# Kernel tuning notes

Measured on AMD Instinct MI355X. Metric: run time of the kernel, lower is better.

Reference implementation:

```python
import jax, jax.numpy as jnp
import numpy as np

N, E = 50000, 800000
NFEAT, NHID, NCLASS = 512, 256, 64
RRELU_SLOPE = (1.0 / 8.0 + 1.0 / 3.0) / 2.0  # nn.RReLU eval-mode negative slope


def spmm(row, col, val, X):
    # sparse adj (COO: row, col, val) @ dense X -> [N, F]
    return jax.ops.segment_sum(X[col] * val[:, None], row, num_segments=N)


def setup_inputs() -> dict:
    key = jax.random.key(0)
    ks = jax.random.split(key, 12)
    x = jax.random.normal(ks[0], (N, NFEAT), dtype=jnp.float32)
    edge_row = jnp.sort(jax.random.randint(ks[1], (E,), 0, N))
    edge_col = jax.random.randint(ks[2], (E,), 0, N)
    # normalized-ish positive adjacency values
    edge_val = jax.random.uniform(ks[3], (E,), dtype=jnp.float32) / 16.0
    def glorot(k, fi, fo):
        s = 1.0 / np.sqrt(fi)
        return jax.random.normal(k, (fi, fo), dtype=jnp.float32) * s
    w1 = glorot(ks[4], NFEAT, NHID)
    b1 = jax.random.normal(ks[5], (NHID,), dtype=jnp.float32) * 0.01
    w2 = glorot(ks[6], NFEAT, NHID)
    b2 = jax.random.normal(ks[7], (NHID,), dtype=jnp.float32) * 0.01
    w3 = glorot(ks[8], NHID, NCLASS)
    b3 = jax.random.normal(ks[9], (NCLASS,), dtype=jnp.float32) * 0.01
    w4 = glorot(ks[10], NFEAT, NCLASS)
    b4 = jax.random.normal(ks[11], (NCLASS,), dtype=jnp.float32) * 0.01
    return {"x": x, "edge_row": edge_row, "edge_col": edge_col, "edge_val": edge_val,
            "w1": w1, "b1": b1, "w2": w2, "b2": b2, "w3": w3, "b3": b3, "w4": w4, "b4": b4}


def reference(x, edge_row, edge_col, edge_val, w1, b1, w2, b2, w3, b3, w4, b4):
    # skip branches (no adj): support = x @ W + b; dropout is identity in eval
    a_skip0 = x @ w2 + b2                                   # [N, NHID]
    a_skip1 = x @ w4 + b4                                   # [N, NCLASS]
    # gc1 with adj
    h1 = spmm(edge_row, edge_col, edge_val, x @ w1) + b1    # [N, NHID]
    v = h1 + a_skip0
    h = jnp.where(v >= 0, v, v * RRELU_SLOPE)               # RReLU (eval mode)
    # gc3 with adj
    out = spmm(edge_row, edge_col, edge_val, h @ w3) + b3 + a_skip1  # [N, NCLASS]
    return (out, w1, w2, w3, w4)
```

## Files before the change

kernel.cpp:

```cpp
#include <hip/hip_runtime.h>

#define N_NODES 50000
#define N_EDGES 800000
#define NFEAT 512
#define NHID 256
#define NCLASS 64
#define NCOMB 576
#define NPAD 640
#define NSKIP 320
#define RRELU_SLOPE 0.2291666666666667f

typedef __attribute__((ext_vector_type(8))) short bf16x8;
typedef __attribute__((ext_vector_type(4))) float f32x4;
typedef __attribute__((ext_vector_type(2))) float f32x2;

#define GLOAD_LDS16(g, l)                                                      \
    __builtin_amdgcn_global_load_lds(                                          \
        (const __attribute__((address_space(1))) void*)(g),                    \
        (__attribute__((address_space(3))) void*)(l), 16, 0, 0)

__device__ __forceinline__ unsigned short f2bf(float f) {
    unsigned int x = __float_as_uint(f);
    unsigned int r = (x + 0x7fffu + ((x >> 16) & 1u)) >> 16;
    return (unsigned short)r;
}
__device__ __forceinline__ float bf2f(unsigned short u) {
    return __uint_as_float(((unsigned int)u) << 16);
}
__device__ __forceinline__ float bf_lo(unsigned int u) { return __uint_as_float(u << 16); }
__device__ __forceinline__ float bf_hi(unsigned int u) { return __uint_as_float(u & 0xffff0000u); }
__device__ __forceinline__ unsigned char f2fp8(float v) {
    return (unsigned char)__builtin_amdgcn_cvt_pk_fp8_f32(v, v, 0, false);
}

#define P_BT 327680
#define P_TOT 328320
#define PK_BLK 1283
#define XC_BLK 2048
#define XC_N 6400000

__global__ __launch_bounds__(256)
void prep(const float* __restrict__ x, const float* __restrict__ w1,
          const float* __restrict__ w2, const float* __restrict__ w4,
          const float* __restrict__ b1, const float* __restrict__ b2,
          const float* __restrict__ b3, const float* __restrict__ b4,
          unsigned short* __restrict__ xb, unsigned short* __restrict__ Bt,
          float* __restrict__ biasb) {
    int b = blockIdx.x;
    if (b < PK_BLK) {
        int i = b * 256 + threadIdx.x;
        if (i < P_BT) {
            int c = i >> 9;
            int k = i & 511;
            float v = 0.f;
            if (c < NHID)            v = w1[k * NHID + c];
            else if (c < 2 * NHID)   v = w2[k * NHID + (c - NHID)];
            else if (c < NCOMB)      v = w4[k * NCLASS + (c - 2 * NHID)];
            Bt[i] = f2bf(v);
        } else if (i < P_TOT) {
            int bb = i - P_BT;
            float v = 0.f;
            if (bb >= NHID && bb < 2 * NHID)       v = b1[bb - NHID] + b2[bb - NHID];
            else if (bb >= 2 * NHID && bb < NCOMB) v = b3[bb - 2 * NHID] + b4[bb - 2 * NHID];
            biasb[bb] = v;
        }
        return;
    }
    for (int i = (b - PK_BLK) * 256 + threadIdx.x; i < XC_N; i += XC_BLK * 256) {
        float4 v = ((const float4*)x)[i];
        ushort4 o;
        o.x = f2bf(v.x); o.y = f2bf(v.y); o.z = f2bf(v.z); o.w = f2bf(v.w);
        ((ushort4*)xb)[i] = o;
    }
}

#define GBM 128
#define GBK 64
#define NCB0 5
#define NRP0 392
#define T0 800000
#define T1 850001
#define T2 866385
#define T3 944209
#define TAIL_BLOCKS ((T3 + 255) / 256)

__global__ __launch_bounds__(256, 4)
void gemm_bf16(const unsigned short* __restrict__ A,
               const unsigned short* __restrict__ Bt,
               const float* __restrict__ bias,
               unsigned char* __restrict__ C8,
               unsigned short* __restrict__ skipb,
               int M, int K,
               const int* __restrict__ erow, const int* __restrict__ ecol,
               const float* __restrict__ ev, const float* __restrict__ w1f,
               const float* __restrict__ w2f, const float* __restrict__ w3f,
               const float* __restrict__ w4f, uint2* __restrict__ ep,
               int* __restrict__ rp, unsigned short* __restrict__ w3t,
               float* __restrict__ outw) {
    __shared__ unsigned short As[GBM * GBK];
    __shared__ unsigned short Bs[128 * GBK];
    int row0, col0;
    {
        int b = blockIdx.x;
        if (b >= NRP0 * NCB0) {
            int i = (b - NRP0 * NCB0) * 256 + threadIdx.x;
            if (i < T0) {
                uint2 e;
                e.x = (unsigned)ecol[i];
                e.y = __float_as_uint(ev[i]);
                ep[i] = e;
            } else if (i < T1) {
                int n = i - T0;
                int lo = 0, hi = N_EDGES;
                while (lo < hi) {
                    int mid = (lo + hi) >> 1;
                    if (erow[mid] < n) lo = mid + 1; else hi = mid;
                }
                rp[n] = lo;
            } else if (i < T2) {
                int j = i - T1;
                int c = j >> 8;
                int k = j & 255;
                w3t[j] = f2bf(w3f[k * NCLASS + c]);
            } else if (i < T3) {
                int j = i - T2;
                float4* o4 = (float4*)outw;
                if (j < 32768)        o4[800000 + j] = ((const float4*)w1f)[j];
                else if (j < 65536)   o4[832768 + (j - 32768)] = ((const float4*)w2f)[j - 32768];
                else if (j < 69632)   o4[865536 + (j - 65536)] = ((const float4*)w3f)[j - 65536];
                else                  o4[869632 + (j - 69632)] = ((const float4*)w4f)[j - 69632];
            }
            return;
        }
        int g = b / (8 * NCB0);
        int w = b % (8 * NCB0);
        int r = g * 8 + (w & 7);
        int c = w >> 3;
        if (r * GBM >= M) return;
        row0 = r * GBM;
        col0 = c * 128;
    }
    const int tid  = threadIdx.x;
    const int lane = tid & 63;
    const int wave = tid >> 6;
    const int wr = (wave >> 1) * 64;
    const int wc = (wave & 1) * 64;
    const int lm = lane & 15;
    const int l4 = lane >> 4;
    const int sw = lm & 7;

    const int sub  = lane >> 3;
    const int slot = lane & 7;
    const int goct = slot ^ sub;

    f32x4 acc[4][4] = {};

    for (int k0 = 0; k0 < K; k0 += GBK) {
        #pragma unroll
        for (int p = 0; p < 4; ++p) {
            int chunk = wave * 4 + p;
            int gr = row0 + chunk * 8 + sub;
            if (gr > M - 1) gr = M - 1;
            GLOAD_LDS16(A + (size_t)gr * K + k0 + goct * 8, As + chunk * 512);
        }
        #pragma unroll
        for (int p = 0; p < 4; ++p) {
            int chunk = wave * 4 + p;
            int rb = col0 + chunk * 8 + sub;
            GLOAD_LDS16(Bt + (size_t)rb * K + k0 + goct * 8, Bs + chunk * 512);
        }
        __syncthreads();

        #pragma unroll
        for (int kk8 = 0; kk8 < GBK / 8; kk8 += 4) {
            const int so = ((kk8 + l4) ^ sw) * 8;
            bf16x8 bfr[4];
            #pragma unroll
            for (int j = 0; j < 4; ++j)
                bfr[j] = *(const bf16x8*)(Bs + (wc + j * 16 + lm) * 64 + so);
            #pragma unroll
            for (int i = 0; i < 4; ++i) {
                bf16x8 af = *(const bf16x8*)(As + (wr + i * 16 + lm) * 64 + so);
                #pragma unroll
                for (int j = 0; j < 4; ++j)
                    acc[i][j] = __builtin_amdgcn_mfma_f32_16x16x32_bf16(af, bfr[j], acc[i][j], 0, 0, 0);
            }
        }
        __syncthreads();
    }

    #pragma unroll
    for (int i = 0; i < 4; ++i) {
        #pragma unroll
        for (int j = 0; j < 4; ++j) {
            int col = col0 + wc + j * 16 + lm;
            float bvv = bias[col];
            #pragma unroll
            for (int r = 0; r < 4; ++r) {
                int row = row0 + wr + i * 16 + l4 * 4 + r;
                if (row < M) {
                    float v = acc[i][j][r];
                    if (col < NHID)       C8[(size_t)row * NHID + col] = f2fp8(v);
                    else if (col < NCOMB) skipb[(size_t)row * NSKIP + (col - NHID)] = f2bf(v + bvv);
                }
            }
        }
    }
}

__global__ __launch_bounds__(256)
void spmm1_rrelu_w3(const int* __restrict__ rp, const uint2* __restrict__ ep,
                    const unsigned char* __restrict__ xw1q,
                    const unsigned short* __restrict__ skipb,
                    const unsigned short* __restrict__ w3t,
                    unsigned char* __restrict__ hw3q, int n_nodes) {
    __shared__ unsigned short hs[16 * 256];
    const int tid = threadIdx.x;
    const int nb = blockIdx.x * 8;
    {
        uint4 z = {0u, 0u, 0u, 0u};
        ((uint4*)hs)[tid] = z;
        ((uint4*)hs)[256 + tid] = z;
    }
    __syncthreads();

    const int row = tid >> 5;
    const int n = nb + row;
    const int l = tid & 31;
    const int f = l * 8;
    if (n < n_nodes) {
        int lo = rp[n], hi = rp[n + 1];
        float s0 = 0.f, s1 = 0.f, s2 = 0.f, s3 = 0.f;
        float s4 = 0.f, s5 = 0.f, s6 = 0.f, s7 = 0.f;
        for (int e = lo; e < hi; e += 8) {
            uint2 ed[8];
            uint2 p[8];
            #pragma unroll
            for (int q = 0; q < 8; ++q) {
                int idx = (e + q < hi) ? e + q : hi - 1;
                ed[q] = ep[idx];
            }
            #pragma unroll
            for (int q = 0; q < 8; ++q)
                p[q] = *(const uint2*)(xw1q + (size_t)ed[q].x * NHID + f);
            #pragma unroll
            for (int q = 0; q < 8; ++q) {
                float v = (e + q < hi) ? __uint_as_float(ed[q].y) : 0.f;
                f32x2 ab = __builtin_amdgcn_cvt_pk_f32_fp8((int)p[q].x, false);
                f32x2 cd = __builtin_amdgcn_cvt_pk_f32_fp8((int)p[q].x, true);
                f32x2 ef = __builtin_amdgcn_cvt_pk_f32_fp8((int)p[q].y, false);
                f32x2 gh = __builtin_amdgcn_cvt_pk_f32_fp8((int)p[q].y, true);
                s0 += v * ab.x; s1 += v * ab.y;
                s2 += v * cd.x; s3 += v * cd.y;
                s4 += v * ef.x; s5 += v * ef.y;
                s6 += v * gh.x; s7 += v * gh.y;
            }
        }
        uint4 sk = *(const uint4*)(skipb + (size_t)n * NSKIP + f);
        float v0 = s0 + bf_lo(sk.x), v1 = s1 + bf_hi(sk.x);
        float v2 = s2 + bf_lo(sk.y), v3 = s3 + bf_hi(sk.y);
        float v4 = s4 + bf_lo(sk.z), v5 = s5 + bf_hi(sk.z);
        float v6 = s6 + bf_lo(sk.w), v7 = s7 + bf_hi(sk.w);
        v0 = (v0 >= 0.f) ? v0 : v0 * RRELU_SLOPE;
        v1 = (v1 >= 0.f) ? v1 : v1 * RRELU_SLOPE;
        v2 = (v2 >= 0.f) ? v2 : v2 * RRELU_SLOPE;
        v3 = (v3 >= 0.f) ? v3 : v3 * RRELU_SLOPE;
        v4 = (v4 >= 0.f) ? v4 : v4 * RRELU_SLOPE;
        v5 = (v5 >= 0.f) ? v5 : v5 * RRELU_SLOPE;
        v6 = (v6 >= 0.f) ? v6 : v6 * RRELU_SLOPE;
        v7 = (v7 >= 0.f) ? v7 : v7 * RRELU_SLOPE;
        uint4 o;
        o.x = (unsigned)f2bf(v0) | ((unsigned)f2bf(v1) << 16);
        o.y = (unsigned)f2bf(v2) | ((unsigned)f2bf(v3) << 16);
        o.z = (unsigned)f2bf(v4) | ((unsigned)f2bf(v5) << 16);
        o.w = (unsigned)f2bf(v6) | ((unsigned)f2bf(v7) << 16);
        ((uint4*)hs)[row * 32 + (l ^ (row & 7))] = o;
    }
    __syncthreads();

    const int lane = tid & 63;
    const int wave = tid >> 6;
    const int lm = lane & 15;
    const int l4 = lane >> 4;
    const int col = wave * 16 + lm;
    const unsigned short* wrow = w3t + (size_t)col * 256;
    f32x4 acc = {};
    #pragma unroll
    for (int s = 0; s < 8; ++s) {
        bf16x8 bfr = *(const bf16x8*)(wrow + s * 32 + l4 * 8);
        int oct = (s * 4 + l4) ^ (lm & 7);
        bf16x8 af = *(const bf16x8*)(hs + lm * 256 + oct * 8);
        acc = __builtin_amdgcn_mfma_f32_16x16x32_bf16(af, bfr, acc, 0, 0, 0);
    }
    #pragma unroll
    for (int r = 0; r < 4; ++r) {
        int orow = l4 * 4 + r;
        int n2 = nb + orow;
        if (orow < 8 && n2 < n_nodes)
            hw3q[(size_t)n2 * NCLASS + col] = f2fp8(acc[r]);
    }
}

__global__ __launch_bounds__(256)
void spmm2_out(const int* __restrict__ rp, const uint2* __restrict__ ep,
               const unsigned char* __restrict__ hw3q,
               const unsigned short* __restrict__ skipb,
               float* __restrict__ out, int n_nodes) {
    int n = blockIdx.x * 8 + (threadIdx.x >> 5);
    if (n >= n_nodes) return;
    int l = threadIdx.x & 31;
    int oct = l >> 3;
    int f = (l & 7) * 8;
    int lo = rp[n], hi = rp[n + 1];
    float s0 = 0.f, s1 = 0.f, s2 = 0.f, s3 = 0.f;
    float s4 = 0.f, s5 = 0.f, s6 = 0.f, s7 = 0.f;
    for (int e = lo + oct; e < hi; e += 8) {
        int i1 = (e + 4 < hi) ? e + 4 : hi - 1;
        uint2 ea = ep[e], eb = ep[i1];
        uint2 pa = *(const uint2*)(hw3q + (size_t)ea.x * NCLASS + f);
        uint2 pb = *(const uint2*)(hw3q + (size_t)eb.x * NCLASS + f);
        float va = __uint_as_float(ea.y);
        float vb = (e + 4 < hi) ? __uint_as_float(eb.y) : 0.f;
        f32x2 a0 = __builtin_amdgcn_cvt_pk_f32_fp8((int)pa.x, false);
        f32x2 a1 = __builtin_amdgcn_cvt_pk_f32_fp8((int)pa.x, true);
        f32x2 a2 = __builtin_amdgcn_cvt_pk_f32_fp8((int)pa.y, false);
        f32x2 a3 = __builtin_amdgcn_cvt_pk_f32_fp8((int)pa.y, true);
        f32x2 b0 = __builtin_amdgcn_cvt_pk_f32_fp8((int)pb.x, false);
        f32x2 b1 = __builtin_amdgcn_cvt_pk_f32_fp8((int)pb.x, true);
        f32x2 b2 = __builtin_amdgcn_cvt_pk_f32_fp8((int)pb.y, false);
        f32x2 b3 = __builtin_amdgcn_cvt_pk_f32_fp8((int)pb.y, true);
        s0 += va * a0.x + vb * b0.x;
        s1 += va * a0.y + vb * b0.y;
        s2 += va * a1.x + vb * b1.x;
        s3 += va * a1.y + vb * b1.y;
        s4 += va * a2.x + vb * b2.x;
        s5 += va * a2.y + vb * b2.y;
        s6 += va * a3.x + vb * b3.x;
        s7 += va * a3.y + vb * b3.y;
    }
    s0 += __shfl_xor(s0, 8); s0 += __shfl_xor(s0, 16);
    s1 += __shfl_xor(s1, 8); s1 += __shfl_xor(s1, 16);
    s2 += __shfl_xor(s2, 8); s2 += __shfl_xor(s2, 16);
    s3 += __shfl_xor(s3, 8); s3 += __shfl_xor(s3, 16);
    s4 += __shfl_xor(s4, 8); s4 += __shfl_xor(s4, 16);
    s5 += __shfl_xor(s5, 8); s5 += __shfl_xor(s5, 16);
    s6 += __shfl_xor(s6, 8); s6 += __shfl_xor(s6, 16);
    s7 += __shfl_xor(s7, 8); s7 += __shfl_xor(s7, 16);
    if (oct == 0) {
        uint4 sv = *(const uint4*)(skipb + (size_t)n * NSKIP + NHID + f);
        float4 o1, o2;
        o1.x = s0 + bf_lo(sv.x); o1.y = s1 + bf_hi(sv.x);
        o1.z = s2 + bf_lo(sv.y); o1.w = s3 + bf_hi(sv.y);
        o2.x = s4 + bf_lo(sv.z); o2.y = s5 + bf_hi(sv.z);
        o2.z = s6 + bf_lo(sv.w); o2.w = s7 + bf_hi(sv.w);
        float4* op = (float4*)(out + (size_t)n * NCLASS + f);
        op[0] = o1;
        op[1] = o2;
    }
}

extern "C" void kernel_launch(void* const* d_in, const int* in_sizes, int n_in,
                              void* d_out, int out_size, void* d_ws, size_t ws_size,
                              hipStream_t stream) {
    const float* x    = (const float*)d_in[0];
    const int*   erow = (const int*)d_in[1];
    const int*   ecol = (const int*)d_in[2];
    const float* ev   = (const float*)d_in[3];
    const float* w1   = (const float*)d_in[4];
    const float* b1   = (const float*)d_in[5];
    const float* w2   = (const float*)d_in[6];
    const float* b2   = (const float*)d_in[7];
    const float* w3   = (const float*)d_in[8];
    const float* b3   = (const float*)d_in[9];
    const float* w4   = (const float*)d_in[10];
    const float* b4   = (const float*)d_in[11];
    float* out = (float*)d_out;

    char* ws = (char*)d_ws;
    size_t off = 0;
    auto alloc = [&](size_t bytes) -> void* {
        off = (off + 255) & ~(size_t)255;
        void* p = ws + off;
        off += bytes;
        return p;
    };

    unsigned short* xb    = (unsigned short*)alloc((size_t)N_NODES * NFEAT * 2);
    unsigned short* Bt    = (unsigned short*)alloc((size_t)NFEAT * NPAD * 2);
    float*          biasb = (float*)alloc(NPAD * 4);
    unsigned char*  xw1q  = (unsigned char*)alloc((size_t)N_NODES * NHID);
    unsigned short* skipb = (unsigned short*)alloc((size_t)N_NODES * NSKIP * 2);
    unsigned short* w3t   = (unsigned short*)alloc((size_t)NHID * NCLASS * 2);
    unsigned char*  hw3q  = (unsigned char*)alloc((size_t)N_NODES * NCLASS);
    int*            rp    = (int*)alloc((size_t)(N_NODES + 1) * 4);
    uint2*          ep    = (uint2*)alloc((size_t)N_EDGES * 8);

    prep<<<PK_BLK + XC_BLK, 256, 0, stream>>>(x, w1, w2, w4, b1, b2, b3, b4,
                                              xb, Bt, biasb);

    gemm_bf16<<<NRP0 * NCB0 + TAIL_BLOCKS, 256, 0, stream>>>(
        xb, Bt, biasb, xw1q, skipb, N_NODES, NFEAT,
        erow, ecol, ev, w1, w2, w3, w4, ep, rp, w3t, out);

    spmm1_rrelu_w3<<<(N_NODES + 7) / 8, 256, 0, stream>>>(
        rp, ep, xw1q, skipb, w3t, hw3q, N_NODES);

    spmm2_out<<<(N_NODES + 7) / 8, 256, 0, stream>>>(rp, ep, hw3q, skipb, out, N_NODES);
}
```

Before: 321.3 us.

## Split spmm1 into feature-quarter gather pass and separate tiled W3 GEMM

The fp8 X@W1 output is stored in four 64-column slabs so each gather row is 64 bytes, and spmm1 now runs a grid over node × quarter with per-wave edge splitting and shuffle reduction. The fused per-block W3 MFMA is moved to a separate LDS-tiled GEMM kernel reading a new bf16 hidden buffer. This targets gather locality and better MFMA utilization, but adds an extra 25 MB bf16 intermediate write/read and one more kernel launch.

```diff
diff --git a/kernel.cpp b/kernel.cpp
--- a/kernel.cpp
+++ b/kernel.cpp
@@ -200,8 +200,11 @@
                 int row = row0 + wr + i * 16 + l4 * 4 + r;
                 if (row < M) {
                     float v = acc[i][j][r];
-                    if (col < NHID)       C8[(size_t)row * NHID + col] = f2fp8(v);
-                    else if (col < NCOMB) skipb[(size_t)row * NSKIP + (col - NHID)] = f2bf(v + bvv);
+                    if (col < NHID) {
+                        C8[((size_t)(col >> 6) * N_NODES + row) * 64 + (col & 63)] = f2fp8(v);
+                    } else if (col < NCOMB) {
+                        skipb[(size_t)row * NSKIP + (col - NHID)] = f2bf(v + bvv);
+                    }
                 }
             }
         }
@@ -209,95 +212,126 @@
 }
 
 __global__ __launch_bounds__(256)
-void spmm1_rrelu_w3(const int* __restrict__ rp, const uint2* __restrict__ ep,
-                    const unsigned char* __restrict__ xw1q,
-                    const unsigned short* __restrict__ skipb,
-                    const unsigned short* __restrict__ w3t,
-                    unsigned char* __restrict__ hw3q, int n_nodes) {
-    __shared__ unsigned short hs[16 * 256];
-    const int tid = threadIdx.x;
-    const int nb = blockIdx.x * 8;
-    {
-        uint4 z = {0u, 0u, 0u, 0u};
-        ((uint4*)hs)[tid] = z;
-        ((uint4*)hs)[256 + tid] = z;
-    }
-    __syncthreads();
-
-    const int row = tid >> 5;
-    const int n = nb + row;
-    const int l = tid & 31;
-    const int f = l * 8;
-    if (n < n_nodes) {
-        int lo = rp[n], hi = rp[n + 1];
-        float s0 = 0.f, s1 = 0.f, s2 = 0.f, s3 = 0.f;
-        float s4 = 0.f, s5 = 0.f, s6 = 0.f, s7 = 0.f;
-        for (int e = lo; e < hi; e += 8) {
-            uint2 ed[8];
-            uint2 p[8];
-            #pragma unroll
-            for (int q = 0; q < 8; ++q) {
-                int idx = (e + q < hi) ? e + q : hi - 1;
-                ed[q] = ep[idx];
-            }
-            #pragma unroll
-            for (int q = 0; q < 8; ++q)
-                p[q] = *(const uint2*)(xw1q + (size_t)ed[q].x * NHID + f);
-            #pragma unroll
-            for (int q = 0; q < 8; ++q) {
-                float v = (e + q < hi) ? __uint_as_float(ed[q].y) : 0.f;
-                f32x2 ab = __builtin_amdgcn_cvt_pk_f32_fp8((int)p[q].x, false);
-                f32x2 cd = __builtin_amdgcn_cvt_pk_f32_fp8((int)p[q].x, true);
-                f32x2 ef = __builtin_amdgcn_cvt_pk_f32_fp8((int)p[q].y, false);
-                f32x2 gh = __builtin_amdgcn_cvt_pk_f32_fp8((int)p[q].y, true);
-                s0 += v * ab.x; s1 += v * ab.y;
-                s2 += v * cd.x; s3 += v * cd.y;
-                s4 += v * ef.x; s5 += v * ef.y;
-                s6 += v * gh.x; s7 += v * gh.y;
-            }
-        }
-        uint4 sk = *(const uint4*)(skipb + (size_t)n * NSKIP + f);
-        float v0 = s0 + bf_lo(sk.x), v1 = s1 + bf_hi(sk.x);
-        float v2 = s2 + bf_lo(sk.y), v3 = s3 + bf_hi(sk.y);
-        float v4 = s4 + bf_lo(sk.z), v5 = s5 + bf_hi(sk.z);
-        float v6 = s6 + bf_lo(sk.w), v7 = s7 + bf_hi(sk.w);
+void spmm1_rrelu(const int* __restrict__ rp, const uint2* __restrict__ ep,
+                 const unsigned char* __restrict__ xw1q,
+                 const unsigned short* __restrict__ skipb,
+                 unsigned short* __restrict__ hbq,
+                 int n_nodes) {
+    int n = blockIdx.x * 4 + (threadIdx.x >> 6);
+    if (n >= n_nodes) return;
+    const int qt = blockIdx.y;
+    const unsigned char* xq = xw1q + (size_t)qt * N_NODES * 64;
+    int lane = threadIdx.x & 63;
+    int q = lane >> 4;
+    int l = lane & 15;
+    int f = l * 4;
+    int lo = rp[n], hi = rp[n + 1];
+    float s0 = 0.f, s1 = 0.f, s2 = 0.f, s3 = 0.f;
+    for (int e = lo + q; e < hi; e += 8) {
+        int i1 = (e + 4 < hi) ? e + 4 : hi - 1;
+        uint2 ea = ep[e], eb = ep[i1];
+        unsigned pa = *(const unsigned*)(xq + (size_t)ea.x * 64 + f);
+        unsigned pb = *(const unsigned*)(xq + (size_t)eb.x * 64 + f);
+        float va = __uint_as_float(ea.y);
+        float vb = (e + 4 < hi) ? __uint_as_float(eb.y) : 0.f;
+        f32x2 a0 = __builtin_amdgcn_cvt_pk_f32_fp8((int)pa, false);
+        f32x2 a1 = __builtin_amdgcn_cvt_pk_f32_fp8((int)pa, true);
+        f32x2 b0 = __builtin_amdgcn_cvt_pk_f32_fp8((int)pb, false);
+        f32x2 b1 = __builtin_amdgcn_cvt_pk_f32_fp8((int)pb, true);
+        s0 += va * a0.x + vb * b0.x;
+        s1 += va * a0.y + vb * b0.y;
+        s2 += va * a1.x + vb * b1.x;
+        s3 += va * a1.y + vb * b1.y;
+    }
+    s0 += __shfl_xor(s0, 16); s0 += __shfl_xor(s0, 32);
+    s1 += __shfl_xor(s1, 16); s1 += __shfl_xor(s1, 32);
+    s2 += __shfl_xor(s2, 16); s2 += __shfl_xor(s2, 32);
+    s3 += __shfl_xor(s3, 16); s3 += __shfl_xor(s3, 32);
+    if (q == 0) {
+        uint2 sv = *(const uint2*)(skipb + (size_t)n * NSKIP + qt * 64 + f);
+        float v0 = s0 + bf_lo(sv.x), v1 = s1 + bf_hi(sv.x);
+        float v2 = s2 + bf_lo(sv.y), v3 = s3 + bf_hi(sv.y);
         v0 = (v0 >= 0.f) ? v0 : v0 * RRELU_SLOPE;
         v1 = (v1 >= 0.f) ? v1 : v1 * RRELU_SLOPE;
         v2 = (v2 >= 0.f) ? v2 : v2 * RRELU_SLOPE;
         v3 = (v3 >= 0.f) ? v3 : v3 * RRELU_SLOPE;
-        v4 = (v4 >= 0.f) ? v4 : v4 * RRELU_SLOPE;
-        v5 = (v5 >= 0.f) ? v5 : v5 * RRELU_SLOPE;
-        v6 = (v6 >= 0.f) ? v6 : v6 * RRELU_SLOPE;
-        v7 = (v7 >= 0.f) ? v7 : v7 * RRELU_SLOPE;
-        uint4 o;
+        uint2 o;
         o.x = (unsigned)f2bf(v0) | ((unsigned)f2bf(v1) << 16);
         o.y = (unsigned)f2bf(v2) | ((unsigned)f2bf(v3) << 16);
-        o.z = (unsigned)f2bf(v4) | ((unsigned)f2bf(v5) << 16);
-        o.w = (unsigned)f2bf(v6) | ((unsigned)f2bf(v7) << 16);
-        ((uint4*)hs)[row * 32 + (l ^ (row & 7))] = o;
-    }
-    __syncthreads();
-
+        *(uint2*)(hbq + ((size_t)qt * N_NODES + n) * 64 + f) = o;
+    }
+}
+
+__global__ __launch_bounds__(256, 4)
+void gemm1(const unsigned short* __restrict__ hbq,
+           const unsigned short* __restrict__ w3t,
+           unsigned char* __restrict__ hw3q,
+           int M) {
+    __shared__ unsigned short As[GBM * GBK];
+    __shared__ unsigned short Bs[64 * GBK];
+    const int row0 = blockIdx.x * GBM;
+    const int tid  = threadIdx.x;
     const int lane = tid & 63;
     const int wave = tid >> 6;
+    const int wr = (wave >> 1) * 64;
+    const int wc = (wave & 1) * 32;
     const int lm = lane & 15;
     const int l4 = lane >> 4;
-    const int col = wave * 16 + lm;
-    const unsigned short* wrow = w3t + (size_t)col * 256;
-    f32x4 acc = {};
+    const int sw = lm & 7;
+
+    const int sub  = lane >> 3;
+    const int slot = lane & 7;
+    const int goct = slot ^ sub;
+
+    f32x4 acc[4][2] = {};
+
+    for (int t = 0; t < 4; ++t) {
+        const unsigned short* Aq = hbq + (size_t)t * N_NODES * 64;
+        #pragma unroll
+        for (int p = 0; p < 4; ++p) {
+            int chunk = wave * 4 + p;
+            int gr = row0 + chunk * 8 + sub;
+            if (gr > M - 1) gr = M - 1;
+            GLOAD_LDS16(Aq + (size_t)gr * 64 + goct * 8, As + chunk * 512);
+        }
+        #pragma unroll
+        for (int p = 0; p < 2; ++p) {
+            int chunk = wave * 2 + p;
+            int rb = chunk * 8 + sub;
+            GLOAD_LDS16(w3t + (size_t)rb * 256 + t * 64 + goct * 8, Bs + chunk * 512);
+        }
+        __syncthreads();
+
+        #pragma unroll
+        for (int kk8 = 0; kk8 < 8; kk8 += 4) {
+            const int so = ((kk8 + l4) ^ sw) * 8;
+            bf16x8 bfr[2];
+            #pragma unroll
+            for (int j = 0; j < 2; ++j)
+                bfr[j] = *(const bf16x8*)(Bs + (wc + j * 16 + lm) * 64 + so);
+            #pragma unroll
+            for (int i = 0; i < 4; ++i) {
+                bf16x8 af = *(const bf16x8*)(As + (wr + i * 16 + lm) * 64 + so);
+                #pragma unroll
+                for (int j = 0; j < 2; ++j)
+                    acc[i][j] = __builtin_amdgcn_mfma_f32_16x16x32_bf16(af, bfr[j], acc[i][j], 0, 0, 0);
+            }
+        }
+        __syncthreads();
+    }
+
     #pragma unroll
-    for (int s = 0; s < 8; ++s) {
-        bf16x8 bfr = *(const bf16x8*)(wrow + s * 32 + l4 * 8);
-        int oct = (s * 4 + l4) ^ (lm & 7);
-        bf16x8 af = *(const bf16x8*)(hs + lm * 256 + oct * 8);
-        acc = __builtin_amdgcn_mfma_f32_16x16x32_bf16(af, bfr, acc, 0, 0, 0);
-    }
-    #pragma unroll
-    for (int r = 0; r < 4; ++r) {
-        int orow = l4 * 4 + r;
-        int n2 = nb + orow;
-        if (orow < 8 && n2 < n_nodes)
-            hw3q[(size_t)n2 * NCLASS + col] = f2fp8(acc[r]);
+    for (int i = 0; i < 4; ++i) {
+        #pragma unroll
+        for (int j = 0; j < 2; ++j) {
+            int col = wc + j * 16 + lm;
+            #pragma unroll
+            for (int r = 0; r < 4; ++r) {
+                int row = row0 + wr + i * 16 + l4 * 4 + r;
+                if (row < M)
+                    hw3q[(size_t)row * NCLASS + col] = f2fp8(acc[i][j][r]);
+            }
+        }
     }
 }
 
@@ -390,6 +424,7 @@
     float*          biasb = (float*)alloc(NPAD * 4);
     unsigned char*  xw1q  = (unsigned char*)alloc((size_t)N_NODES * NHID);
     unsigned short* skipb = (unsigned short*)alloc((size_t)N_NODES * NSKIP * 2);
+    unsigned short* hbq   = (unsigned short*)alloc((size_t)N_NODES * NHID * 2);
     unsigned short* w3t   = (unsigned short*)alloc((size_t)NHID * NCLASS * 2);
     unsigned char*  hw3q  = (unsigned char*)alloc((size_t)N_NODES * NCLASS);
     int*            rp    = (int*)alloc((size_t)(N_NODES + 1) * 4);
@@ -402,8 +437,10 @@
         xb, Bt, biasb, xw1q, skipb, N_NODES, NFEAT,
         erow, ecol, ev, w1, w2, w3, w4, ep, rp, w3t, out);
 
-    spmm1_rrelu_w3<<<(N_NODES + 7) / 8, 256, 0, stream>>>(
-        rp, ep, xw1q, skipb, w3t, hw3q, N_NODES);
+    dim3 g1((N_NODES + 3) / 4, 4);
+    spmm1_rrelu<<<g1, 256, 0, stream>>>(rp, ep, xw1q, skipb, hbq, N_NODES);
+
+    gemm1<<<(N_NODES + GBM - 1) / GBM, 256, 0, stream>>>(hbq, w3t, hw3q, N_NODES);
 
     spmm2_out<<<(N_NODES + 7) / 8, 256, 0, stream>>>(rp, ep, hw3q, skipb, out, N_NODES);
 }
```

Measured after the change: 341.2 us. 1.06x slower.
